# Optimization experiments

Hardware: AMD Instinct MI355X
Metric: run time of the kernel (lower is better)

## Reference

```python
import jax, jax.numpy as jnp
import numpy as np

B, T, H, L = 16384, 100, 32, 6  # batch voxels, time frames, hidden, layers


def setup_inputs() -> dict:
    key = jax.random.key(0)
    ks = jax.random.split(key, 12)
    s = 0.1  # small init scale akin to PyTorch's uniform(-1/sqrt(H), 1/sqrt(H))
    F = L * H  # 192, head input dim
    return {
        "x": jax.random.normal(ks[0], (B, T, 1), jnp.float32),
        "W_ih0": jax.random.normal(ks[1], (3 * H, 1), jnp.float32) * s,   # layer 0 input weights
        "W_ih": jax.random.normal(ks[2], (L - 1, 3 * H, H), jnp.float32) * s,  # layers 1..5
        "W_hh": jax.random.normal(ks[3], (L, 3 * H, H), jnp.float32) * s,
        "b_ih": jax.random.normal(ks[4], (L, 3 * H), jnp.float32) * s,
        "b_hh": jax.random.normal(ks[5], (L, 3 * H), jnp.float32) * s,
        "Wk": jax.random.normal(ks[6], (1, F), jnp.float32) * s,
        "bk": jax.random.normal(ks[7], (1,), jnp.float32) * s,
        "We": jax.random.normal(ks[8], (1, F), jnp.float32) * s,
        "be": jax.random.normal(ks[9], (1,), jnp.float32) * s,
        "Wt": jax.random.normal(ks[10], (1, F), jnp.float32) * s,
        "bt": jax.random.normal(ks[11], (1,), jnp.float32) * s,
    }


def _gru_layer(x_seq, Wi, Wh, bi, bh):
    # x_seq: [T, B, D_in]; gate order (r, z, n) matches torch.nn.GRU
    xw = jnp.einsum('tbd,gd->tbg', x_seq, Wi) + bi  # precompute input projections [T,B,3H]

    def step(h, xw_t):
        hg = h @ Wh.T + bh                      # [B, 3H]
        xr, xz, xn = jnp.split(xw_t, 3, axis=-1)
        hr, hz, hn = jnp.split(hg, 3, axis=-1)
        r = jax.nn.sigmoid(xr + hr)
        z = jax.nn.sigmoid(xz + hz)
        n = jnp.tanh(xn + r * hn)
        h_new = (1.0 - z) * n + z * h
        return h_new, h_new

    h0 = jnp.zeros((x_seq.shape[1], Wh.shape[1]), x_seq.dtype)
    h_last, out = jax.lax.scan(step, h0, xw)
    return out, h_last


def reference(x, W_ih0, W_ih, W_hh, b_ih, b_hh, Wk, bk, We, be, Wt, bt):
    seq = jnp.transpose(x, (1, 0, 2))  # [T, B, 1] (time-major for scan)
    finals = []
    seq, h_last = _gru_layer(seq, W_ih0, W_hh[0], b_ih[0], b_hh[0])
    finals.append(h_last)
    for l in range(1, L):
        seq, h_last = _gru_layer(seq, W_ih[l - 1], W_hh[l], b_ih[l], b_hh[l])
        finals.append(h_last)
    # rearrange 'l n h -> n (l h)'
    feat = jnp.transpose(jnp.stack(finals), (1, 0, 2)).reshape(x.shape[0], L * H)
    ktrans = feat @ Wk.T + bk
    kep = feat @ We.T + be
    t0 = feat @ Wt.T + bt
    return (ktrans, kep, t0)
```

## Files before the change

### kernel.cpp

```cpp
#include <hip/hip_runtime.h>

#define T_LEN 100
#define H 32
#define L 6
#define NT 6
#define TPB 512
#define BT 32
#define NPAIR 25
#define NK (NPAIR + L - 1)
#define S1 1.44269504088896f

typedef float f32x4  __attribute__((ext_vector_type(4)));
typedef _Float16 f16x8 __attribute__((ext_vector_type(8)));

union FragU { f16x8 h; f32x4 f; unsigned int u[4]; };

__device__ inline unsigned short f2h(float f) {
    union { _Float16 h; unsigned short u; } v; v.h = (_Float16)f; return v.u;
}
__device__ inline float rcpa(float x)  { return __builtin_amdgcn_rcpf(x); }
__device__ inline float exp2b(float x) { return __builtin_amdgcn_exp2f(x); }

__device__ inline unsigned int pk16(float a, float b) {
    unsigned int h;
    asm("v_cvt_pkrtz_f16_f32 %0, %1, %2" : "=v"(h) : "v"(a), "v"(b));
    return h;
}

__global__ void pack_frags(const float* __restrict__ Whh, const float* __restrict__ Wih,
                           unsigned short* __restrict__ WhFhi,
                           unsigned short* __restrict__ WiFhi)
{
    int tid = blockIdx.x * blockDim.x + threadIdx.x;
    const int NWH = L * NT * 64;
    const int NWI = (L - 1) * NT * 64;
    if (tid >= NWH + NWI) return;
    const float* src; unsigned short *dhi; int tile, lane;
    if (tid < NWH) {
        int l = tid / (NT * 64); int r = tid % (NT * 64); tile = r / 64; lane = r % 64;
        src = Whh + l * 96 * H;
        dhi = WhFhi + tid * 8;
    } else {
        int t2 = tid - NWH;
        int l = t2 / (NT * 64); int r = t2 % (NT * 64); tile = r / 64; lane = r % 64;
        src = Wih + l * 96 * H;
        dhi = WiFhi + t2 * 8;
    }
    int row = tile * 16 + (lane & 15);
    int gk  = lane >> 4;
    float scale = (row < 64) ? -S1 : -2.0f * S1;
    unsigned short thi[8];
#pragma unroll
    for (int e = 0; e < 8; ++e) {
        int j = ((e >> 2) << 4) + (gk << 2) + (e & 3);
        thi[e] = f2h(scale * src[row * H + j]);
    }
    *(uint4*)dhi = *(const uint4*)thi;
}

__global__ __launch_bounds__(TPB, 2) void gru_mfma(
    const float* __restrict__ x,
    const float* __restrict__ Wih0,
    const float* __restrict__ bih,
    const float* __restrict__ bhh,
    const unsigned short* __restrict__ WhFhi,
    const unsigned short* __restrict__ WiFhi,
    const float* __restrict__ Wk, const float* __restrict__ bk,
    const float* __restrict__ We, const float* __restrict__ be,
    const float* __restrict__ Wt, const float* __restrict__ bt,
    float* __restrict__ out, int B)
{
    __shared__ unsigned char slot[5][2][4][2048];
    __shared__ float xt[T_LEN][BT];
    __shared__ float hpart[L][3][BT];

    const int tid  = threadIdx.x;
    const int wv   = tid >> 6;
    const int lane = tid & 63;
    const int b    = lane & 15;
    const int g    = lane >> 4;
    const int b0   = blockIdx.x * BT;

    int layer, grmask;
    switch (wv) {
      case 0: layer = 0; grmask = 3; break;
      case 4: layer = 1; grmask = 1; break;
      case 1: layer = 2; grmask = 3; break;
      case 5: layer = 1; grmask = 2; break;
      case 2: layer = 3; grmask = 3; break;
      case 6: layer = 5; grmask = 1; break;
      case 3: layer = 4; grmask = 3; break;
      default: layer = 5; grmask = 2; break;
    }

    for (int idx = tid; idx < T_LEN * BT; idx += TPB) {
        int bb = idx / T_LEN, t = idx % T_LEN;
        xt[t][bb] = x[(b0 + bb) * T_LEN + t];
    }

    f16x8 whh[NT], wih[NT];
#pragma unroll
    for (int t6 = 0; t6 < NT; ++t6)
        whh[t6] = ((const f16x8*)WhFhi)[(layer * NT + t6) * 64 + lane];
    if (layer > 0) {
#pragma unroll
        for (int t6 = 0; t6 < NT; ++t6)
            wih[t6] = ((const f16x8*)WiFhi)[((layer - 1) * NT + t6) * 64 + lane];
    }

    f32x4 bc[4], bxn[2], bhn[2];
    {
        const int rb = g * 4;
#pragma unroll
        for (int t6 = 0; t6 < 4; ++t6)
#pragma unroll
            for (int r = 0; r < 4; ++r) {
                int row = t6 * 16 + rb + r;
                bc[t6][r] = -S1 * (bih[layer * 96 + row] + bhh[layer * 96 + row]);
            }
#pragma unroll
        for (int tt = 0; tt < 2; ++tt)
#pragma unroll
            for (int r = 0; r < 4; ++r) {
                int row = 64 + tt * 16 + rb + r;
                bxn[tt][r] = -2.0f * S1 * bih[layer * 96 + row];
                bhn[tt][r] = -2.0f * S1 * bhh[layer * 96 + row];
            }
        if (layer == 0) {
#pragma unroll
            for (int t6 = 0; t6 < NT; ++t6) {
                FragU u;
#pragma unroll
                for (int r = 0; r < 4; ++r) {
                    int row = t6 * 16 + rb + r;
                    float s = (row < 64) ? -S1 : -2.0f * S1;
                    u.f[r] = s * Wih0[row];
                }
                wih[t6] = u.h;
            }
        }
    }

    float hp[2][8];
#pragma unroll
    for (int gr = 0; gr < 2; ++gr)
#pragma unroll
        for (int i = 0; i < 8; ++i) hp[gr][i] = 0.0f;
    f16x8 hfH[2] = {{0,0,0,0,0,0,0,0},{0,0,0,0,0,0,0,0}};

    const int soff = b * 64 + ((g ^ ((b >> 1) & 3)) << 4);
    unsigned char* const sbase = (unsigned char*)slot;

    auto do_step2 = [&](int t, int rq, int wp, int st) {
        f32x4 acc[2][4], accX[2][2], accH[2][2];
        f16x8 iH[2];
        if (layer > 0) {
            const unsigned char* ru = sbase + (((layer - 1) * 8 + rq * 4 + st) << 11);
            if (grmask & 1) iH[0] = *(const f16x8*)(ru + soff);
            if (grmask & 2) iH[1] = *(const f16x8*)(ru + 1024 + soff);
        }
#pragma unroll
        for (int gr = 0; gr < 2; ++gr)
            if (grmask & (1 << gr)) {
#pragma unroll
                for (int t6 = 0; t6 < 4; ++t6)
                    acc[gr][t6] = __builtin_amdgcn_mfma_f32_16x16x32_f16(whh[t6], hfH[gr], bc[t6], 0, 0, 0);
#pragma unroll
                for (int tt = 0; tt < 2; ++tt)
                    accH[gr][tt] = __builtin_amdgcn_mfma_f32_16x16x32_f16(whh[4 + tt], hfH[gr], bhn[tt], 0, 0, 0);
            }
        if (layer == 0) {
#pragma unroll
            for (int gr = 0; gr < 2; ++gr)
                if (grmask & (1 << gr)) {
                    float xv = xt[t][gr * 16 + b];
#pragma unroll
                    for (int t6 = 0; t6 < 4; ++t6) {
                        FragU u; u.h = wih[t6];
#pragma unroll
                        for (int r = 0; r < 4; ++r)
                            acc[gr][t6][r] = fmaf(u.f[r], xv, acc[gr][t6][r]);
                    }
#pragma unroll
                    for (int tt = 0; tt < 2; ++tt) {
                        FragU u; u.h = wih[4 + tt];
#pragma unroll
                        for (int r = 0; r < 4; ++r)
                            accX[gr][tt][r] = fmaf(u.f[r], xv, bxn[tt][r]);
                    }
                }
        } else {
#pragma unroll
            for (int gr = 0; gr < 2; ++gr)
                if (grmask & (1 << gr)) {
#pragma unroll
                    for (int t6 = 0; t6 < 4; ++t6)
                        acc[gr][t6] = __builtin_amdgcn_mfma_f32_16x16x32_f16(wih[t6], iH[gr], acc[gr][t6], 0, 0, 0);
#pragma unroll
                    for (int tt = 0; tt < 2; ++tt)
                        accX[gr][tt] = __builtin_amdgcn_mfma_f32_16x16x32_f16(wih[4 + tt], iH[gr], bxn[tt], 0, 0, 0);
                }
        }
#pragma unroll
        for (int gr = 0; gr < 2; ++gr)
            if (grmask & (1 << gr)) {
#pragma unroll
                for (int jj = 0; jj < 2; ++jj)
#pragma unroll
                    for (int r = 0; r < 4; ++r) {
                        float Er = exp2b(acc[gr][jj][r]);
                        float Ez = exp2b(acc[gr][2 + jj][r]);
                        float rg = rcpa(1.0f + Er);
                        float u  = fmaf(rg, accH[gr][jj][r], accX[gr][jj][r]);
                        float En = exp2b(u);
                        float en1 = 1.0f + En, ez1 = 1.0f + Ez;
                        float d   = rcpa(en1 * ez1);
                        float num = fmaf(hp[gr][jj * 4 + r], en1, (1.0f - En) * Ez);
                        hp[gr][jj * 4 + r] = num * d;
                    }
            }
#pragma unroll
        for (int gr = 0; gr < 2; ++gr)
            if (grmask & (1 << gr)) {
                unsigned int h01 = pk16(hp[gr][0], hp[gr][1]);
                unsigned int h23 = pk16(hp[gr][2], hp[gr][3]);
                unsigned int h45 = pk16(hp[gr][4], hp[gr][5]);
                unsigned int h67 = pk16(hp[gr][6], hp[gr][7]);
                FragU Hu;
                Hu.u[0] = h01; Hu.u[1] = h23; Hu.u[2] = h45; Hu.u[3] = h67;
                hfH[gr] = Hu.h;
                if (layer < L - 1) {
                    unsigned char* wp8 = sbase + ((layer * 8 + wp * 4 + st) << 11) + gr * 1024;
                    *(uint4*)(wp8 + soff) = make_uint4(h01, h23, h45, h67);
                }
            }
    };

    __syncthreads();

    for (int i = 0; i < NK; ++i) {
        int k = i - layer;
        if (0 <= k && k < NPAIR) {
            const int p = i & 1, q = p ^ 1;
#pragma unroll
            for (int st = 0; st < 4; ++st)
                do_step2(4 * k + st, q, p, st);
        }
        __syncthreads();
    }

    {
        const int rb = g * 4;
#pragma unroll
        for (int hd = 0; hd < 3; ++hd) {
            const float* W = (hd == 0) ? Wk : (hd == 1) ? We : Wt;
#pragma unroll
            for (int gr = 0; gr < 2; ++gr)
                if (grmask & (1 << gr)) {
                    float s = 0.0f;
#pragma unroll
                    for (int jj = 0; jj < 2; ++jj)
#pragma unroll
                        for (int r = 0; r < 4; ++r)
                            s = fmaf(W[layer * H + jj * 16 + rb + r], hp[gr][jj * 4 + r], s);
                    s += __shfl_xor(s, 16, 64);
                    s += __shfl_xor(s, 32, 64);
                    if (g == 0) hpart[layer][hd][gr * 16 + b] = s;
                }
        }
        __syncthreads();
        if (wv < 3 && lane < BT) {
            int bb = lane;
            float s = (wv == 0) ? bk[0] : (wv == 1) ? be[0] : bt[0];
#pragma unroll
            for (int l = 0; l < L; ++l) s += hpart[l][wv][bb];
            out[wv * B + b0 + bb] = s;
        }
    }
}

extern "C" void kernel_launch(void* const* d_in, const int* in_sizes, int n_in,
                              void* d_out, int out_size, void* d_ws, size_t ws_size,
                              hipStream_t stream)
{
    const float* x    = (const float*)d_in[0];
    const float* Wih0 = (const float*)d_in[1];
    const float* Wih  = (const float*)d_in[2];
    const float* Whh  = (const float*)d_in[3];
    const float* bih  = (const float*)d_in[4];
    const float* bhh  = (const float*)d_in[5];
    const float* Wk   = (const float*)d_in[6];
    const float* bk   = (const float*)d_in[7];
    const float* We   = (const float*)d_in[8];
    const float* be   = (const float*)d_in[9];
    const float* Wt   = (const float*)d_in[10];
    const float* bt   = (const float*)d_in[11];
    float* out = (float*)d_out;

    const int B = in_sizes[0] / T_LEN;

    unsigned short* WhFhi = (unsigned short*)d_ws;
    unsigned short* WiFhi = WhFhi + L * NT * 64 * 8;

    const int nPack = (L * NT * 64) + ((L - 1) * NT * 64);
    pack_frags<<<(nPack + 255) / 256, 256, 0, stream>>>(Whh, Wih, WhFhi, WiFhi);
    gru_mfma<<<B / BT, TPB, 0, stream>>>(x, Wih0, bih, bhh, WhFhi, WiFhi,
                                         Wk, bk, We, be, Wt, bt, out, B);
}
```

Baseline: 244.1 us.

## Software-pipeline GRU steps by prefetching next step's input projection during gates

New measurement: 259.0 us. 6.1% more time.

```diff
diff --git a/kernel.cpp b/kernel.cpp
--- a/kernel.cpp
+++ b/kernel.cpp
@@ -151,25 +151,30 @@
     const int soff = b * 64 + ((g ^ ((b >> 1) & 3)) << 4);
     unsigned char* const sbase = (unsigned char*)slot;
 
-    auto do_step2 = [&](int t, int rq, int wp, int st) {
-        f32x4 acc[2][4], accX[2][2], accH[2][2];
-        f16x8 iH[2];
+
+    auto fill = [&](f32x4 (&A)[2][8], int t, int rq, int st) {
         if (layer > 0) {
             const unsigned char* ru = sbase + (((layer - 1) * 8 + rq * 4 + st) << 11);
-            if (grmask & 1) iH[0] = *(const f16x8*)(ru + soff);
-            if (grmask & 2) iH[1] = *(const f16x8*)(ru + 1024 + soff);
-        }
-#pragma unroll
-        for (int gr = 0; gr < 2; ++gr)
-            if (grmask & (1 << gr)) {
+            f16x8 iH0, iH1;
+            if (grmask & 1) iH0 = *(const f16x8*)(ru + soff);
+            if (grmask & 2) iH1 = *(const f16x8*)(ru + 1024 + soff);
+            if (grmask & 1) {
 #pragma unroll
                 for (int t6 = 0; t6 < 4; ++t6)
-                    acc[gr][t6] = __builtin_amdgcn_mfma_f32_16x16x32_f16(whh[t6], hfH[gr], bc[t6], 0, 0, 0);
+                    A[0][t6] = __builtin_amdgcn_mfma_f32_16x16x32_f16(wih[t6], iH0, bc[t6], 0, 0, 0);
 #pragma unroll
                 for (int tt = 0; tt < 2; ++tt)
-                    accH[gr][tt] = __builtin_amdgcn_mfma_f32_16x16x32_f16(whh[4 + tt], hfH[gr], bhn[tt], 0, 0, 0);
-            }
-        if (layer == 0) {
+                    A[0][4 + tt] = __builtin_amdgcn_mfma_f32_16x16x32_f16(wih[4 + tt], iH0, bxn[tt], 0, 0, 0);
+            }
+            if (grmask & 2) {
+#pragma unroll
+                for (int t6 = 0; t6 < 4; ++t6)
+                    A[1][t6] = __builtin_amdgcn_mfma_f32_16x16x32_f16(wih[t6], iH1, bc[t6], 0, 0, 0);
+#pragma unroll
+                for (int tt = 0; tt < 2; ++tt)
+                    A[1][4 + tt] = __builtin_amdgcn_mfma_f32_16x16x32_f16(wih[4 + tt], iH1, bxn[tt], 0, 0, 0);
+            }
+        } else {
 #pragma unroll
             for (int gr = 0; gr < 2; ++gr)
                 if (grmask & (1 << gr)) {
@@ -179,49 +184,51 @@
                         FragU u; u.h = wih[t6];
 #pragma unroll
                         for (int r = 0; r < 4; ++r)
-                            acc[gr][t6][r] = fmaf(u.f[r], xv, acc[gr][t6][r]);
+                            A[gr][t6][r] = fmaf(u.f[r], xv, bc[t6][r]);
                     }
 #pragma unroll
                     for (int tt = 0; tt < 2; ++tt) {
                         FragU u; u.h = wih[4 + tt];
 #pragma unroll
                         for (int r = 0; r < 4; ++r)
-                            accX[gr][tt][r] = fmaf(u.f[r], xv, bxn[tt][r]);
+                            A[gr][4 + tt][r] = fmaf(u.f[r], xv, bxn[tt][r]);
                     }
                 }
-        } else {
-#pragma unroll
-            for (int gr = 0; gr < 2; ++gr)
-                if (grmask & (1 << gr)) {
-#pragma unroll
-                    for (int t6 = 0; t6 < 4; ++t6)
-                        acc[gr][t6] = __builtin_amdgcn_mfma_f32_16x16x32_f16(wih[t6], iH[gr], acc[gr][t6], 0, 0, 0);
-#pragma unroll
-                    for (int tt = 0; tt < 2; ++tt)
-                        accX[gr][tt] = __builtin_amdgcn_mfma_f32_16x16x32_f16(wih[4 + tt], iH[gr], bxn[tt], 0, 0, 0);
-                }
-        }
+        }
+    };
+
+    auto ownh = [&](f32x4 (&A)[2][8]) {
 #pragma unroll
         for (int gr = 0; gr < 2; ++gr)
             if (grmask & (1 << gr)) {
 #pragma unroll
+                for (int t6 = 0; t6 < 4; ++t6)
+                    A[gr][t6] = __builtin_amdgcn_mfma_f32_16x16x32_f16(whh[t6], hfH[gr], A[gr][t6], 0, 0, 0);
+#pragma unroll
+                for (int tt = 0; tt < 2; ++tt)
+                    A[gr][6 + tt] = __builtin_amdgcn_mfma_f32_16x16x32_f16(whh[4 + tt], hfH[gr], bhn[tt], 0, 0, 0);
+            }
+    };
+
+    auto gates = [&](f32x4 (&A)[2][8], int wp, int st) {
+#pragma unroll
+        for (int gr = 0; gr < 2; ++gr)
+            if (grmask & (1 << gr)) {
+#pragma unroll
                 for (int jj = 0; jj < 2; ++jj)
 #pragma unroll
                     for (int r = 0; r < 4; ++r) {
-                        float Er = exp2b(acc[gr][jj][r]);
-                        float Ez = exp2b(acc[gr][2 + jj][r]);
+                        float Er = exp2b(A[gr][jj][r]);
+                        float Ez = exp2b(A[gr][2 + jj][r]);
                         float rg = rcpa(1.0f + Er);
-                        float u  = fmaf(rg, accH[gr][jj][r], accX[gr][jj][r]);
+                        float u  = fmaf(rg, A[gr][6 + jj][r], A[gr][4 + jj][r]);
                         float En = exp2b(u);
                         float en1 = 1.0f + En, ez1 = 1.0f + Ez;
                         float d   = rcpa(en1 * ez1);
-                        float num = fmaf(hp[gr][jj * 4 + r], en1, (1.0f - En) * Ez);
+                        float t2  = fmaf(-En, Ez, Ez);
+                        float num = fmaf(hp[gr][jj * 4 + r], en1, t2);
                         hp[gr][jj * 4 + r] = num * d;
                     }
-            }
-#pragma unroll
-        for (int gr = 0; gr < 2; ++gr)
-            if (grmask & (1 << gr)) {
                 unsigned int h01 = pk16(hp[gr][0], hp[gr][1]);
                 unsigned int h23 = pk16(hp[gr][2], hp[gr][3]);
                 unsigned int h45 = pk16(hp[gr][4], hp[gr][5]);
@@ -236,15 +243,20 @@
             }
     };
 
+    f32x4 A0[2][8], A1[2][8];
+
     __syncthreads();
 
     for (int i = 0; i < NK; ++i) {
         int k = i - layer;
         if (0 <= k && k < NPAIR) {
             const int p = i & 1, q = p ^ 1;
-#pragma unroll
-            for (int st = 0; st < 4; ++st)
-                do_step2(4 * k + st, q, p, st);
+            const int t0 = 4 * k;
+            fill(A0, t0 + 0, q, 0);
+            ownh(A0); fill(A1, t0 + 1, q, 1); gates(A0, p, 0);
+            ownh(A1); fill(A0, t0 + 2, q, 2); gates(A1, p, 1);
+            ownh(A0); fill(A1, t0 + 3, q, 3); gates(A0, p, 2);
+            ownh(A1);                         gates(A1, p, 3);
         }
         __syncthreads();
     }
```
